# Performance work log

Hardware: AMD Instinct MI355X
Metric: run time of the kernel (lower is better)

## Reference

```python
import jax, jax.numpy as jnp
import numpy as np

V, E, H, C = 50257, 256, 512, 16  # vocab, embed_dim, hidden_size, n_cells
B, T = 256, 128
LN_EPS = 1e-5


def setup_inputs() -> dict:
    key = jax.random.key(0)
    ks = jax.random.split(key, 16)
    s_h = 1.0 / np.sqrt(H)
    s_e = 1.0 / np.sqrt(E)
    return {
        "tokens": jax.random.randint(ks[0], (B, T), 0, V),
        "emb": jax.random.normal(ks[1], (V, E), jnp.float32) * 0.02,
        "Wproj": jax.random.normal(ks[2], (E, H), jnp.float32) * s_e,
        "bproj": jnp.zeros((H,), jnp.float32),
        "Wp": jax.random.normal(ks[3], (C, H, H), jnp.float32) * s_h,
        "bp": jnp.zeros((C, H), jnp.float32),
        "ln_g": jnp.ones((C, H), jnp.float32),
        "ln_b": jnp.zeros((C, H), jnp.float32),
        "Wih": jax.random.normal(ks[4], (C, 4 * H, H), jnp.float32) * s_h,
        "bih": jnp.zeros((C, 4 * H), jnp.float32),
        "Whh": jax.random.normal(ks[5], (C, 4 * H, H), jnp.float32) * s_h,
        "bhh": jnp.zeros((C, 4 * H), jnp.float32),
        "Wa": jax.random.normal(ks[6], (C, H, H), jnp.float32) * s_h,
        "ba": jnp.zeros((C, H), jnp.float32),
        "gate_logit": jnp.zeros((C,), jnp.float32),  # torch.tensor(0.0) per cell
    }


def _layernorm(x, g, b):
    mu = jnp.mean(x, axis=-1, keepdims=True)
    var = jnp.var(x, axis=-1, keepdims=True)
    return (x - mu) * jax.lax.rsqrt(var + LN_EPS) * g + b


def reference(tokens, emb, Wproj, bproj, Wp, bp, ln_g, ln_b,
              Wih, bih, Whh, bhh, Wa, ba, gate_logit):
    # embedding (padding_idx=0 zeroed) + projection to hidden size
    emb = emb.at[0].set(0.0)
    xs = emb[tokens] @ Wproj + bproj              # [B,T,H]
    xs = jnp.transpose(xs, (1, 0, 2))             # [T,B,H] for scan

    gate = jax.nn.sigmoid(gate_logit)[:, None, None]  # [C,1,1]

    def step(carry, x_t):
        h, c, ext = carry                          # h,c: [C,B,H], ext: [B,H]
        # input_adapter == Identity (input_size == hidden_size); external injection
        x = x_t[None] + 0.3 * ext[None]            # [C,B,H]
        # perception: Linear + ReLU + LayerNorm
        p = jax.nn.relu(jnp.einsum('cbh,chk->cbk', x, Wp) + bp[:, None, :])
        p = _layernorm(p, ln_g[:, None, :], ln_b[:, None, :])
        # LSTMCell (torch gate order i, f, g, o)
        gates = (jnp.einsum('cbh,cgh->cbg', p, Wih) + bih[:, None, :]
                 + jnp.einsum('cbh,cgh->cbg', h, Whh) + bhh[:, None, :])
        i_g, f_g, g_g, o_g = jnp.split(gates, 4, axis=-1)
        c_new = jax.nn.sigmoid(f_g) * c + jax.nn.sigmoid(i_g) * jnp.tanh(g_g)
        h_new = jax.nn.sigmoid(o_g) * jnp.tanh(c_new)
        # association + sigmoid gate
        a = jnp.tanh(jnp.einsum('cbh,chk->cbk', h_new, Wa) + ba[:, None, :])
        out = a * gate                             # [C,B,H]
        y = jnp.mean(out, axis=0)                  # aggregate cells -> [B,H]
        return (h_new, c_new, y), y

    h0 = jnp.zeros((C, B, H), xs.dtype)
    c0 = jnp.zeros((C, B, H), xs.dtype)
    ext0 = jnp.zeros((B, H), xs.dtype)
    _, ys = jax.lax.scan(step, (h0, c0, ext0), xs)  # ys: [T,B,H]
    return jnp.transpose(ys, (1, 0, 2))             # [B,T,H]
```

## Files before the change

kernel.cpp:

```cpp
#include <hip/hip_runtime.h>
#include <hip/hip_bf16.h>

#define V 50257
#define E 256
#define H 512
#define C 16
#define B 256
#define T 128

typedef _Float16 f16x8 __attribute__((ext_vector_type(8)));
typedef _Float16 f16x4 __attribute__((ext_vector_type(4)));
typedef float f32x4 __attribute__((ext_vector_type(4)));

__device__ __forceinline__ float sigm(float x) { return 1.0f / (1.0f + __expf(-x)); }

__device__ __forceinline__ void gload16(const _Float16* g, _Float16* l) {
  __builtin_amdgcn_global_load_lds((const __attribute__((address_space(1))) unsigned*)g,
                                   (__attribute__((address_space(3))) unsigned*)l, 16, 0, 0);
}

__global__ __launch_bounds__(256) void k_emb(const int* __restrict__ tokens,
                                             const float* __restrict__ emb,
                                             const float* __restrict__ Wproj,
                                             const float* __restrict__ bproj,
                                             _Float16* __restrict__ xs_h) {
  __shared__ float elds[16][256];
  const int tid = threadIdx.x;
  const int r0 = blockIdx.x * 16;
#pragma unroll
  for (int i = 0; i < 16; ++i) {
    int r = r0 + i;
    int t = r >> 8, b = r & 255;
    int tok = tokens[b * T + t];
    elds[i][tid] = (tok == 0) ? 0.0f : emb[(size_t)tok * E + tid];
  }
  __syncthreads();
  float acc0[16], acc1[16];
#pragma unroll
  for (int i = 0; i < 16; ++i) { acc0[i] = 0.0f; acc1[i] = 0.0f; }
  for (int k = 0; k < E; k += 4) {
    float w0[4], w1[4];
#pragma unroll
    for (int kk = 0; kk < 4; ++kk) {
      w0[kk] = Wproj[(k + kk) * H + tid];
      w1[kk] = Wproj[(k + kk) * H + tid + 256];
    }
#pragma unroll
    for (int i = 0; i < 16; ++i) {
      float4 e4 = *(const float4*)&elds[i][k];
      acc0[i] = fmaf(e4.x, w0[0], acc0[i]);
      acc0[i] = fmaf(e4.y, w0[1], acc0[i]);
      acc0[i] = fmaf(e4.z, w0[2], acc0[i]);
      acc0[i] = fmaf(e4.w, w0[3], acc0[i]);
      acc1[i] = fmaf(e4.x, w1[0], acc1[i]);
      acc1[i] = fmaf(e4.y, w1[1], acc1[i]);
      acc1[i] = fmaf(e4.z, w1[2], acc1[i]);
      acc1[i] = fmaf(e4.w, w1[3], acc1[i]);
    }
  }
  float bp0 = bproj[tid], bp1 = bproj[tid + 256];
#pragma unroll
  for (int i = 0; i < 16; ++i) {
    size_t r = (size_t)(r0 + i);
    xs_h[r * H + tid] = (_Float16)(acc0[i] + bp0);
    xs_h[r * H + tid + 256] = (_Float16)(acc1[i] + bp1);
  }
}

__global__ __launch_bounds__(256) void k_cvt_wg(const float* __restrict__ Wih,
                                                const float* __restrict__ Whh,
                                                _Float16* __restrict__ WgT) {
  for (size_t i4 = ((size_t)blockIdx.x * 256 + threadIdx.x) * 4; i4 < (size_t)33554432;
       i4 += (size_t)gridDim.x * 1024) {
    size_t c = i4 >> 21;
    size_t rem = i4 & 2097151;
    size_t np = rem >> 10;
    size_t k2 = rem & 1023;
    int gate = (int)((np >> 4) & 3);
    int hh = (int)(((np >> 6) << 4) | (np & 15));
    size_t n = (size_t)gate * 512 + hh;
    const float* src = (k2 < 512) ? (Wih + (c * 2048 + n) * 512 + k2)
                                  : (Whh + (c * 2048 + n) * 512 + (k2 - 512));
    float4 v = *(const float4*)src;
    f16x4 o;
    o[0] = (_Float16)v.x; o[1] = (_Float16)v.y; o[2] = (_Float16)v.z; o[3] = (_Float16)v.w;
    *(f16x4*)&WgT[i4] = o;
  }
}

__global__ __launch_bounds__(256) void k_cvt_tr(const float* __restrict__ W,
                                                _Float16* __restrict__ WT) {
  __shared__ float tl[64][65];
  const int tid = threadIdx.x;
  const int c = blockIdx.z;
  const int k0 = blockIdx.y * 64, n0 = blockIdx.x * 64;
  const float* Wc = W + (size_t)c * 262144;
#pragma unroll
  for (int q = 0; q < 16; ++q) {
    int idx = q * 256 + tid;
    int r = idx >> 6, cc = idx & 63;
    tl[r][cc] = Wc[(size_t)(k0 + r) * 512 + n0 + cc];
  }
  __syncthreads();
  _Float16* WTc = WT + (size_t)c * 262144;
#pragma unroll
  for (int q = 0; q < 16; ++q) {
    int idx = q * 256 + tid;
    int rr = idx >> 6, cc = idx & 63;
    WTc[(size_t)(n0 + rr) * 512 + k0 + cc] = (_Float16)tl[cc][rr];
  }
}

__global__ __launch_bounds__(256) void k_bias(const float* __restrict__ bih,
                                              const float* __restrict__ bhh,
                                              float* __restrict__ bsum) {
  int i = blockIdx.x * 256 + threadIdx.x;
  if (i < C * 4 * H) {
    int c = i >> 11, np = i & 2047;
    int gate = (np >> 4) & 3;
    int hh = ((np >> 6) << 4) | (np & 15);
    int n = gate * 512 + hh;
    bsum[i] = bih[c * 2048 + n] + bhh[c * 2048 + n];
  }
}

template <int EPI, int KK, int LDA, int LDB, int ACS, int BCS, int OLD, int BLD>
__global__ __launch_bounds__(256, 2) void k_gemm(const _Float16* __restrict__ A,
                                                 const _Float16* __restrict__ Bm,
                                                 _Float16* __restrict__ hout,
                                                 const float* __restrict__ bias,
                                                 const float* __restrict__ gl,
                                                 float* __restrict__ cstate,
                                                 _Float16* __restrict__ hdst) {
  __shared__ _Float16 Asl[128 * 64];
  __shared__ _Float16 Bsl[128 * 64];
  const int tid = threadIdx.x;
  const int w = tid >> 6, l = tid & 63;
  const int c = blockIdx.z;
  const int m0 = blockIdx.y * 128, n0 = blockIdx.x * 128;
  const _Float16* Ab = A + (size_t)c * ACS + (size_t)m0 * LDA;
  const _Float16* Bb = Bm + (size_t)c * BCS + (size_t)n0 * LDB;
  f32x4 acc[4][4];
#pragma unroll
  for (int i = 0; i < 4; ++i)
#pragma unroll
    for (int j = 0; j < 4; ++j) acc[i][j] = (f32x4)0.0f;
  const int wm = (w >> 1) * 64, wn = (w & 1) * 64;
  const int srow = l >> 3, sj = l & 7;
#pragma unroll 1
  for (int kb = 0; kb < KK / 64; ++kb) {
#pragma unroll
    for (int q = 0; q < 4; ++q) {
      int r = w * 32 + q * 8 + srow;
      int gj = sj ^ (r & 7);
      gload16(Ab + (size_t)r * LDA + kb * 64 + gj * 8, &Asl[(w * 32 + q * 8) * 64]);
      gload16(Bb + (size_t)r * LDB + kb * 64 + gj * 8, &Bsl[(w * 32 + q * 8) * 64]);
    }
    __syncthreads();
#pragma unroll
    for (int s2 = 0; s2 < 2; ++s2) {
      f16x8 af[4], bf[4];
#pragma unroll
      for (int i = 0; i < 4; ++i) {
        int R = wm + i * 16 + (l & 15);
        int p = (s2 * 4 + (l >> 4)) ^ (R & 7);
        af[i] = *(const f16x8*)&Asl[R * 64 + p * 8];
        int RN = wn + i * 16 + (l & 15);
        int pn = (s2 * 4 + (l >> 4)) ^ (RN & 7);
        bf[i] = *(const f16x8*)&Bsl[RN * 64 + pn * 8];
      }
#pragma unroll
      for (int i = 0; i < 4; ++i)
#pragma unroll
        for (int j = 0; j < 4; ++j)
          acc[i][j] = __builtin_amdgcn_mfma_f32_16x16x32_f16(af[i], bf[j], acc[i][j], 0, 0, 0);
    }
    __syncthreads();
  }
  const int rl = (l >> 4) * 4, cl = l & 15;
  if (EPI == 3) {
    const int hh = (((n0 + wn) >> 6) << 4) + cl;
    float bv[4];
#pragma unroll
    for (int j = 0; j < 4; ++j) bv[j] = bias[(size_t)c * BLD + (n0 + wn) + j * 16 + cl];
#pragma unroll
    for (int i = 0; i < 4; ++i) {
#pragma unroll
      for (int rg = 0; rg < 4; ++rg) {
        int row = m0 + wm + i * 16 + rl + rg;
        float ig = acc[i][0][rg] + bv[0];
        float fg = acc[i][1][rg] + bv[1];
        float gg = acc[i][2][rg] + bv[2];
        float og = acc[i][3][rg] + bv[3];
        size_t ci = ((size_t)c * 256 + row) * 512 + hh;
        float cn = sigm(fg) * cstate[ci] + sigm(ig) * tanhf(gg);
        cstate[ci] = cn;
        hdst[((size_t)c * 256 + row) * 1024 + 512 + hh] = (_Float16)(sigm(og) * tanhf(cn));
      }
    }
  } else {
    float gv = 0.0f;
    if (EPI == 2) gv = sigm(gl[c]);
#pragma unroll
    for (int i = 0; i < 4; ++i) {
#pragma unroll
      for (int j = 0; j < 4; ++j) {
        int gc = n0 + wn + j * 16 + cl;
        float bv = bias[(size_t)c * BLD + gc];
#pragma unroll
        for (int rg = 0; rg < 4; ++rg) {
          int gr = m0 + wm + i * 16 + rl + rg;
          float v = acc[i][j][rg] + bv;
          if (EPI == 0) v = fmaxf(v, 0.0f);
          if (EPI == 2) v = tanhf(v) * gv;
          hout[(size_t)c * (256 * (size_t)OLD) + (size_t)gr * OLD + gc] = (_Float16)v;
        }
      }
    }
  }
}

__global__ __launch_bounds__(256) void k_ln(_Float16* __restrict__ Aq,
                                            const float* __restrict__ g,
                                            const float* __restrict__ b) {
  int row = blockIdx.x * 4 + (threadIdx.x >> 6);
  int l = threadIdx.x & 63;
  int c = row >> 8;
  _Float16* p = Aq + (size_t)row * 1024 + l * 8;
  f16x8 v = *(const f16x8*)p;
  float vf[8];
  float s1 = 0.0f, s2 = 0.0f;
#pragma unroll
  for (int j = 0; j < 8; ++j) {
    vf[j] = (float)v[j];
    s1 += vf[j];
    s2 += vf[j] * vf[j];
  }
#pragma unroll
  for (int m = 1; m < 64; m <<= 1) {
    s1 += __shfl_xor(s1, m, 64);
    s2 += __shfl_xor(s2, m, 64);
  }
  float mu = s1 * (1.0f / 512.0f);
  float var = s2 * (1.0f / 512.0f) - mu * mu;
  float rs = rsqrtf(var + 1e-5f);
  int col0 = l * 8;
#pragma unroll
  for (int j = 0; j < 8; ++j) {
    float o = (vf[j] - mu) * rs * g[c * 512 + col0 + j] + b[c * 512 + col0 + j];
    v[j] = (_Float16)o;
  }
  *(f16x8*)p = v;
}

__global__ __launch_bounds__(256) void k_agg(const _Float16* __restrict__ abuf,
                                             const _Float16* __restrict__ xs_h,
                                             _Float16* __restrict__ xq,
                                             float* __restrict__ out, int t) {
  int idx = blockIdx.x * 256 + threadIdx.x;
  int i4 = idx * 4;
  float s[4] = {0.0f, 0.0f, 0.0f, 0.0f};
#pragma unroll
  for (int c = 0; c < 16; ++c) {
    f16x4 a = *(const f16x4*)&abuf[(size_t)c * 131072 + i4];
#pragma unroll
    for (int j = 0; j < 4; ++j) s[j] += (float)a[j];
  }
  int b = i4 >> 9, h = i4 & 511;
  float4 y4;
  float* yp = &y4.x;
#pragma unroll
  for (int j = 0; j < 4; ++j) yp[j] = s[j] * (1.0f / 16.0f);
  *(float4*)&out[((size_t)b * T + t) * 512 + h] = y4;
  if (t + 1 < T) {
    f16x4 xs4 = *(const f16x4*)&xs_h[(size_t)(t + 1) * 131072 + i4];
    f16x4 xn;
#pragma unroll
    for (int j = 0; j < 4; ++j) xn[j] = (_Float16)((float)xs4[j] + 0.3f * yp[j]);
    *(f16x4*)&xq[i4] = xn;
  }
}

extern "C" void kernel_launch(void* const* d_in, const int* in_sizes, int n_in,
                              void* d_out, int out_size, void* d_ws, size_t ws_size,
                              hipStream_t stream) {
  const int* tokens = (const int*)d_in[0];
  const float* emb = (const float*)d_in[1];
  const float* Wproj = (const float*)d_in[2];
  const float* bproj = (const float*)d_in[3];
  const float* Wp = (const float*)d_in[4];
  const float* bp = (const float*)d_in[5];
  const float* ln_g = (const float*)d_in[6];
  const float* ln_b = (const float*)d_in[7];
  const float* Wih = (const float*)d_in[8];
  const float* bih = (const float*)d_in[9];
  const float* Whh = (const float*)d_in[10];
  const float* bhh = (const float*)d_in[11];
  const float* Wa = (const float*)d_in[12];
  const float* ba = (const float*)d_in[13];
  const float* gl = (const float*)d_in[14];
  float* out = (float*)d_out;

  char* w8 = (char*)d_ws;
  _Float16* xs_h = (_Float16*)w8;
  _Float16* Aq0 = (_Float16*)(w8 + 33554432);
  _Float16* Aq1 = (_Float16*)(w8 + 50331648);
  float* cbuf = (float*)(w8 + 67108864);
  _Float16* abuf = (_Float16*)(w8 + 75497472);
  _Float16* xq = (_Float16*)(w8 + 79691776);
  _Float16* WpT = (_Float16*)(w8 + 79953920);
  _Float16* WaT = (_Float16*)(w8 + 88342528);
  _Float16* WgT = (_Float16*)(w8 + 96731136);
  float* bsum = (float*)(w8 + 163840000);

  hipMemsetAsync(Aq0, 0, 16777216, stream);
  hipMemsetAsync(cbuf, 0, 8388608, stream);

  k_cvt_wg<<<4096, 256, 0, stream>>>(Wih, Whh, WgT);
  k_cvt_tr<<<dim3(8, 8, 16), 256, 0, stream>>>(Wp, WpT);
  k_cvt_tr<<<dim3(8, 8, 16), 256, 0, stream>>>(Wa, WaT);
  k_bias<<<128, 256, 0, stream>>>(bih, bhh, bsum);
  k_emb<<<T * B / 16, 256, 0, stream>>>(tokens, emb, Wproj, bproj, xs_h);
  hipMemcpyAsync(xq, xs_h, 262144, hipMemcpyDeviceToDevice, stream);

  for (int t = 0; t < T; ++t) {
    _Float16* Ac = (t & 1) ? Aq1 : Aq0;
    _Float16* An = (t & 1) ? Aq0 : Aq1;
    k_gemm<0, 512, 512, 512, 0, 262144, 1024, 512>
        <<<dim3(4, 2, 16), 256, 0, stream>>>(xq, WpT, Ac, bp, nullptr, nullptr, nullptr);
    k_ln<<<1024, 256, 0, stream>>>(Ac, ln_g, ln_b);
    k_gemm<3, 1024, 1024, 1024, 262144, 2097152, 1, 2048>
        <<<dim3(16, 2, 16), 256, 0, stream>>>(Ac, WgT, nullptr, bsum, nullptr, cbuf, An);
    k_gemm<2, 512, 1024, 512, 262144, 262144, 512, 512>
        <<<dim3(4, 2, 16), 256, 0, stream>>>(An + 512, WaT, abuf, ba, gl, nullptr, nullptr);
    k_agg<<<128, 256, 0, stream>>>(abuf, xs_h, xq, out, t);
  }
}
```

Baseline: 7.975 ms.

## Fuse LayerNorm into perception GEMM and cell aggregation into association GEMM

Perception now uses one kernel, k_pln. Each block computes a full 32x512 row tile of the ReLU projection and applies LayerNorm in the epilogue: row statistics are reduced with shuffles and shared memory. The association GEMM now does the cross-cell mean, the output write and the next-step input injection. The last block to finish each output tile, tracked by a per-step atomic counter, does this work. Together these cut five launches per timestep to three and remove separate passes over the intermediate buffers. The cost is larger per-block tiles, a threadfence plus atomic handshake, and counters stored in the already-consumed t=0 slice of the embedding buffer.

```diff
diff --git a/kernel.cpp b/kernel.cpp
--- a/kernel.cpp
+++ b/kernel.cpp
@@ -124,22 +124,158 @@
   }
 }
 
-template <int EPI, int KK, int LDA, int LDB, int ACS, int BCS, int OLD, int BLD>
-__global__ __launch_bounds__(256, 2) void k_gemm(const _Float16* __restrict__ A,
-                                                 const _Float16* __restrict__ Bm,
-                                                 _Float16* __restrict__ hout,
-                                                 const float* __restrict__ bias,
-                                                 const float* __restrict__ gl,
-                                                 float* __restrict__ cstate,
-                                                 _Float16* __restrict__ hdst) {
+__global__ __launch_bounds__(256, 2) void k_pln(const _Float16* __restrict__ xq,
+                                                const _Float16* __restrict__ WpT,
+                                                const float* __restrict__ bp,
+                                                const float* __restrict__ ln_g,
+                                                const float* __restrict__ ln_b,
+                                                _Float16* __restrict__ Pdst) {
+  __shared__ _Float16 Bsl[512 * 64];
+  const int tid = threadIdx.x;
+  const int w = tid >> 6, l = tid & 63;
+  const int mt = blockIdx.x;
+  const int c = blockIdx.y;
+  const int m0 = mt * 32;
+  const _Float16* Bb = WpT + (size_t)c * 262144;
+  const int srow = l >> 3, sj = l & 7;
+  const int lm = l & 15, lk = l >> 4;
+  f32x4 acc[2][8];
+#pragma unroll
+  for (int i = 0; i < 2; ++i)
+#pragma unroll
+    for (int j = 0; j < 8; ++j) acc[i][j] = (f32x4)0.0f;
+  const _Float16* pA0 = xq + (size_t)(m0 + lm) * 512 + lk * 8;
+  const _Float16* pA1 = pA0 + 16 * 512;
+  f16x8 a0s0 = *(const f16x8*)pA0;
+  f16x8 a0s1 = *(const f16x8*)(pA0 + 32);
+  f16x8 a1s0 = *(const f16x8*)pA1;
+  f16x8 a1s1 = *(const f16x8*)(pA1 + 32);
+#pragma unroll 1
+  for (int kb = 0; kb < 8; ++kb) {
+#pragma unroll
+    for (int q = 0; q < 16; ++q) {
+      int r = q * 32 + w * 8 + srow;
+      int gj = sj ^ (r & 7);
+      gload16(Bb + (size_t)r * 512 + kb * 64 + gj * 8, &Bsl[(q * 32 + w * 8) * 64]);
+    }
+    f16x8 u00 = a0s0, u01 = a0s1, u10 = a1s0, u11 = a1s1;
+    if (kb < 7) {
+      a0s0 = *(const f16x8*)(pA0 + (kb + 1) * 64);
+      a0s1 = *(const f16x8*)(pA0 + (kb + 1) * 64 + 32);
+      a1s0 = *(const f16x8*)(pA1 + (kb + 1) * 64);
+      a1s1 = *(const f16x8*)(pA1 + (kb + 1) * 64 + 32);
+    }
+    __syncthreads();
+#pragma unroll
+    for (int s2 = 0; s2 < 2; ++s2) {
+      f16x8 bf[8];
+#pragma unroll
+      for (int j = 0; j < 8; ++j) {
+        int RN = w * 128 + j * 16 + lm;
+        int pn = (s2 * 4 + lk) ^ (RN & 7);
+        bf[j] = *(const f16x8*)&Bsl[RN * 64 + pn * 8];
+      }
+      f16x8 ua = s2 ? u01 : u00;
+      f16x8 ub = s2 ? u11 : u10;
+#pragma unroll
+      for (int j = 0; j < 8; ++j) {
+        acc[0][j] = __builtin_amdgcn_mfma_f32_16x16x32_f16(ua, bf[j], acc[0][j], 0, 0, 0);
+        acc[1][j] = __builtin_amdgcn_mfma_f32_16x16x32_f16(ub, bf[j], acc[1][j], 0, 0, 0);
+      }
+    }
+    __syncthreads();
+  }
+  float bv[8], gcol[8], bcol[8];
+#pragma unroll
+  for (int j = 0; j < 8; ++j) {
+    int col = w * 128 + j * 16 + lm;
+    bv[j] = bp[c * 512 + col];
+    gcol[j] = ln_g[c * 512 + col];
+    bcol[j] = ln_b[c * 512 + col];
+  }
+  float vals[2][8][4];
+  float s1l[2][4], s2l[2][4];
+#pragma unroll
+  for (int i = 0; i < 2; ++i)
+#pragma unroll
+    for (int rg = 0; rg < 4; ++rg) { s1l[i][rg] = 0.0f; s2l[i][rg] = 0.0f; }
+#pragma unroll
+  for (int i = 0; i < 2; ++i)
+#pragma unroll
+    for (int j = 0; j < 8; ++j)
+#pragma unroll
+      for (int rg = 0; rg < 4; ++rg) {
+        float v = fmaxf(acc[i][j][rg] + bv[j], 0.0f);
+        vals[i][j][rg] = v;
+        s1l[i][rg] += v;
+        s2l[i][rg] += v * v;
+      }
+#pragma unroll
+  for (int m = 1; m < 16; m <<= 1) {
+#pragma unroll
+    for (int i = 0; i < 2; ++i)
+#pragma unroll
+      for (int rg = 0; rg < 4; ++rg) {
+        s1l[i][rg] += __shfl_xor(s1l[i][rg], m, 64);
+        s2l[i][rg] += __shfl_xor(s2l[i][rg], m, 64);
+      }
+  }
+  float* st = (float*)Bsl;
+  if (lm == 0) {
+#pragma unroll
+    for (int i = 0; i < 2; ++i)
+#pragma unroll
+      for (int rg = 0; rg < 4; ++rg) {
+        int row = i * 16 + lk * 4 + rg;
+        st[(w * 32 + row) * 2] = s1l[i][rg];
+        st[(w * 32 + row) * 2 + 1] = s2l[i][rg];
+      }
+  }
+  __syncthreads();
+  float mu_[2][4], rs_[2][4];
+#pragma unroll
+  for (int i = 0; i < 2; ++i)
+#pragma unroll
+    for (int rg = 0; rg < 4; ++rg) {
+      int row = i * 16 + lk * 4 + rg;
+      float t1 = 0.0f, t2 = 0.0f;
+#pragma unroll
+      for (int ww = 0; ww < 4; ++ww) {
+        t1 += st[(ww * 32 + row) * 2];
+        t2 += st[(ww * 32 + row) * 2 + 1];
+      }
+      float mu = t1 * (1.0f / 512.0f);
+      float var = t2 * (1.0f / 512.0f) - mu * mu;
+      mu_[i][rg] = mu;
+      rs_[i][rg] = rsqrtf(var + 1e-5f);
+    }
+#pragma unroll
+  for (int i = 0; i < 2; ++i)
+#pragma unroll
+    for (int j = 0; j < 8; ++j) {
+      int col = w * 128 + j * 16 + lm;
+#pragma unroll
+      for (int rg = 0; rg < 4; ++rg) {
+        int row = i * 16 + lk * 4 + rg;
+        float o = (vals[i][j][rg] - mu_[i][rg]) * rs_[i][rg] * gcol[j] + bcol[j];
+        Pdst[((size_t)c * 256 + m0 + row) * 1024 + col] = (_Float16)o;
+      }
+    }
+}
+
+__global__ __launch_bounds__(256, 2) void k_gates(const _Float16* __restrict__ A,
+                                                  const _Float16* __restrict__ Bm,
+                                                  const float* __restrict__ bias,
+                                                  float* __restrict__ cstate,
+                                                  _Float16* __restrict__ hdst) {
   __shared__ _Float16 Asl[128 * 64];
   __shared__ _Float16 Bsl[128 * 64];
   const int tid = threadIdx.x;
   const int w = tid >> 6, l = tid & 63;
   const int c = blockIdx.z;
   const int m0 = blockIdx.y * 128, n0 = blockIdx.x * 128;
-  const _Float16* Ab = A + (size_t)c * ACS + (size_t)m0 * LDA;
-  const _Float16* Bb = Bm + (size_t)c * BCS + (size_t)n0 * LDB;
+  const _Float16* Ab = A + (size_t)c * 262144 + (size_t)m0 * 1024;
+  const _Float16* Bb = Bm + (size_t)c * 2097152 + (size_t)n0 * 1024;
   f32x4 acc[4][4];
 #pragma unroll
   for (int i = 0; i < 4; ++i)
@@ -148,13 +284,13 @@
   const int wm = (w >> 1) * 64, wn = (w & 1) * 64;
   const int srow = l >> 3, sj = l & 7;
 #pragma unroll 1
-  for (int kb = 0; kb < KK / 64; ++kb) {
+  for (int kb = 0; kb < 16; ++kb) {
 #pragma unroll
     for (int q = 0; q < 4; ++q) {
       int r = w * 32 + q * 8 + srow;
       int gj = sj ^ (r & 7);
-      gload16(Ab + (size_t)r * LDA + kb * 64 + gj * 8, &Asl[(w * 32 + q * 8) * 64]);
-      gload16(Bb + (size_t)r * LDB + kb * 64 + gj * 8, &Bsl[(w * 32 + q * 8) * 64]);
+      gload16(Ab + (size_t)r * 1024 + kb * 64 + gj * 8, &Asl[(w * 32 + q * 8) * 64]);
+      gload16(Bb + (size_t)r * 1024 + kb * 64 + gj * 8, &Bsl[(w * 32 + q * 8) * 64]);
     }
     __syncthreads();
 #pragma unroll
@@ -178,106 +314,142 @@
     __syncthreads();
   }
   const int rl = (l >> 4) * 4, cl = l & 15;
-  if (EPI == 3) {
-    const int hh = (((n0 + wn) >> 6) << 4) + cl;
-    float bv[4];
-#pragma unroll
-    for (int j = 0; j < 4; ++j) bv[j] = bias[(size_t)c * BLD + (n0 + wn) + j * 16 + cl];
-#pragma unroll
-    for (int i = 0; i < 4; ++i) {
+  const int hh = (((n0 + wn) >> 6) << 4) + cl;
+  float bv[4];
+#pragma unroll
+  for (int j = 0; j < 4; ++j) bv[j] = bias[(size_t)c * 2048 + (n0 + wn) + j * 16 + cl];
+#pragma unroll
+  for (int i = 0; i < 4; ++i) {
+#pragma unroll
+    for (int rg = 0; rg < 4; ++rg) {
+      int row = m0 + wm + i * 16 + rl + rg;
+      float ig = acc[i][0][rg] + bv[0];
+      float fg = acc[i][1][rg] + bv[1];
+      float gg = acc[i][2][rg] + bv[2];
+      float og = acc[i][3][rg] + bv[3];
+      size_t ci = ((size_t)c * 256 + row) * 512 + hh;
+      float cn = sigm(fg) * cstate[ci] + sigm(ig) * tanhf(gg);
+      cstate[ci] = cn;
+      hdst[((size_t)c * 256 + row) * 1024 + 512 + hh] = (_Float16)(sigm(og) * tanhf(cn));
+    }
+  }
+}
+
+__global__ __launch_bounds__(256, 2) void k_assoc(const _Float16* __restrict__ An,
+                                                  const _Float16* __restrict__ WaT,
+                                                  const float* __restrict__ ba,
+                                                  const float* __restrict__ gl,
+                                                  _Float16* __restrict__ abuf,
+                                                  unsigned* __restrict__ cnt,
+                                                  const _Float16* __restrict__ xs_h,
+                                                  _Float16* __restrict__ xq,
+                                                  float* __restrict__ out, int t) {
+  __shared__ _Float16 Asl[64 * 64];
+  __shared__ _Float16 Bsl[128 * 64];
+  __shared__ int lastFlag;
+  const int tid = threadIdx.x;
+  const int w = tid >> 6, l = tid & 63;
+  const int nt = blockIdx.x, mt = blockIdx.y, c = blockIdx.z;
+  const int n0 = nt * 128;
+  const _Float16* Ab = An + 512 + ((size_t)c * 256 + mt * 64) * 1024;
+  const _Float16* Bb = WaT + (size_t)c * 262144 + (size_t)n0 * 512;
+  f32x4 acc[2][4];
+#pragma unroll
+  for (int i = 0; i < 2; ++i)
+#pragma unroll
+    for (int j = 0; j < 4; ++j) acc[i][j] = (f32x4)0.0f;
+  const int wm = (w >> 1) * 32, wn = (w & 1) * 64;
+  const int srow = l >> 3, sj = l & 7;
+  const int lm = l & 15, lk = l >> 4;
+#pragma unroll 1
+  for (int kb = 0; kb < 8; ++kb) {
+#pragma unroll
+    for (int q = 0; q < 2; ++q) {
+      int r = q * 32 + w * 8 + srow;
+      int gj = sj ^ (r & 7);
+      gload16(Ab + (size_t)r * 1024 + kb * 64 + gj * 8, &Asl[(q * 32 + w * 8) * 64]);
+    }
+#pragma unroll
+    for (int q = 0; q < 4; ++q) {
+      int r = q * 32 + w * 8 + srow;
+      int gj = sj ^ (r & 7);
+      gload16(Bb + (size_t)r * 512 + kb * 64 + gj * 8, &Bsl[(q * 32 + w * 8) * 64]);
+    }
+    __syncthreads();
+#pragma unroll
+    for (int s2 = 0; s2 < 2; ++s2) {
+      f16x8 af[2], bf[4];
+#pragma unroll
+      for (int i = 0; i < 2; ++i) {
+        int R = wm + i * 16 + lm;
+        int p = (s2 * 4 + lk) ^ (R & 7);
+        af[i] = *(const f16x8*)&Asl[R * 64 + p * 8];
+      }
+#pragma unroll
+      for (int j = 0; j < 4; ++j) {
+        int RN = wn + j * 16 + lm;
+        int pn = (s2 * 4 + lk) ^ (RN & 7);
+        bf[j] = *(const f16x8*)&Bsl[RN * 64 + pn * 8];
+      }
+#pragma unroll
+      for (int i = 0; i < 2; ++i)
+#pragma unroll
+        for (int j = 0; j < 4; ++j)
+          acc[i][j] = __builtin_amdgcn_mfma_f32_16x16x32_f16(af[i], bf[j], acc[i][j], 0, 0, 0);
+    }
+    __syncthreads();
+  }
+  float gv = sigm(gl[c]);
+#pragma unroll
+  for (int i = 0; i < 2; ++i)
+#pragma unroll
+    for (int j = 0; j < 4; ++j) {
+      int gc = n0 + wn + j * 16 + lm;
+      float bav = ba[c * 512 + gc];
 #pragma unroll
       for (int rg = 0; rg < 4; ++rg) {
-        int row = m0 + wm + i * 16 + rl + rg;
-        float ig = acc[i][0][rg] + bv[0];
-        float fg = acc[i][1][rg] + bv[1];
-        float gg = acc[i][2][rg] + bv[2];
-        float og = acc[i][3][rg] + bv[3];
-        size_t ci = ((size_t)c * 256 + row) * 512 + hh;
-        float cn = sigm(fg) * cstate[ci] + sigm(ig) * tanhf(gg);
-        cstate[ci] = cn;
-        hdst[((size_t)c * 256 + row) * 1024 + 512 + hh] = (_Float16)(sigm(og) * tanhf(cn));
-      }
-    }
-  } else {
-    float gv = 0.0f;
-    if (EPI == 2) gv = sigm(gl[c]);
-#pragma unroll
-    for (int i = 0; i < 4; ++i) {
-#pragma unroll
-      for (int j = 0; j < 4; ++j) {
-        int gc = n0 + wn + j * 16 + cl;
-        float bv = bias[(size_t)c * BLD + gc];
-#pragma unroll
-        for (int rg = 0; rg < 4; ++rg) {
-          int gr = m0 + wm + i * 16 + rl + rg;
-          float v = acc[i][j][rg] + bv;
-          if (EPI == 0) v = fmaxf(v, 0.0f);
-          if (EPI == 2) v = tanhf(v) * gv;
-          hout[(size_t)c * (256 * (size_t)OLD) + (size_t)gr * OLD + gc] = (_Float16)v;
-        }
-      }
-    }
-  }
-}
-
-__global__ __launch_bounds__(256) void k_ln(_Float16* __restrict__ Aq,
-                                            const float* __restrict__ g,
-                                            const float* __restrict__ b) {
-  int row = blockIdx.x * 4 + (threadIdx.x >> 6);
-  int l = threadIdx.x & 63;
-  int c = row >> 8;
-  _Float16* p = Aq + (size_t)row * 1024 + l * 8;
-  f16x8 v = *(const f16x8*)p;
-  float vf[8];
-  float s1 = 0.0f, s2 = 0.0f;
-#pragma unroll
-  for (int j = 0; j < 8; ++j) {
-    vf[j] = (float)v[j];
-    s1 += vf[j];
-    s2 += vf[j] * vf[j];
-  }
-#pragma unroll
-  for (int m = 1; m < 64; m <<= 1) {
-    s1 += __shfl_xor(s1, m, 64);
-    s2 += __shfl_xor(s2, m, 64);
-  }
-  float mu = s1 * (1.0f / 512.0f);
-  float var = s2 * (1.0f / 512.0f) - mu * mu;
-  float rs = rsqrtf(var + 1e-5f);
-  int col0 = l * 8;
-#pragma unroll
-  for (int j = 0; j < 8; ++j) {
-    float o = (vf[j] - mu) * rs * g[c * 512 + col0 + j] + b[c * 512 + col0 + j];
-    v[j] = (_Float16)o;
-  }
-  *(f16x8*)p = v;
-}
-
-__global__ __launch_bounds__(256) void k_agg(const _Float16* __restrict__ abuf,
-                                             const _Float16* __restrict__ xs_h,
-                                             _Float16* __restrict__ xq,
-                                             float* __restrict__ out, int t) {
-  int idx = blockIdx.x * 256 + threadIdx.x;
-  int i4 = idx * 4;
-  float s[4] = {0.0f, 0.0f, 0.0f, 0.0f};
-#pragma unroll
-  for (int c = 0; c < 16; ++c) {
-    f16x4 a = *(const f16x4*)&abuf[(size_t)c * 131072 + i4];
-#pragma unroll
-    for (int j = 0; j < 4; ++j) s[j] += (float)a[j];
-  }
-  int b = i4 >> 9, h = i4 & 511;
-  float4 y4;
-  float* yp = &y4.x;
-#pragma unroll
-  for (int j = 0; j < 4; ++j) yp[j] = s[j] * (1.0f / 16.0f);
-  *(float4*)&out[((size_t)b * T + t) * 512 + h] = y4;
-  if (t + 1 < T) {
-    f16x4 xs4 = *(const f16x4*)&xs_h[(size_t)(t + 1) * 131072 + i4];
-    f16x4 xn;
-#pragma unroll
-    for (int j = 0; j < 4; ++j) xn[j] = (_Float16)((float)xs4[j] + 0.3f * yp[j]);
-    *(f16x4*)&xq[i4] = xn;
+        int row = mt * 64 + wm + i * 16 + lk * 4 + rg;
+        float v = tanhf(acc[i][j][rg] + bav) * gv;
+        abuf[(size_t)c * 131072 + (size_t)row * 512 + gc] = (_Float16)v;
+      }
+    }
+  __threadfence();
+  __syncthreads();
+  if (tid == 0) {
+    unsigned old = atomicAdd(&cnt[t * 16 + mt * 4 + nt], 1u);
+    lastFlag = (old == 15u);
+  }
+  __syncthreads();
+  if (!lastFlag) return;
+  __threadfence();
+  const int br0 = mt * 64;
+#pragma unroll 1
+  for (int rnd = 0; rnd < 4; ++rnd) {
+    int g = rnd * 256 + tid;
+    int row = g >> 4;
+    int colg = (g & 15) * 8;
+    size_t off = (size_t)(br0 + row) * 512 + n0 + colg;
+    float s[8] = {0, 0, 0, 0, 0, 0, 0, 0};
+#pragma unroll
+    for (int cc = 0; cc < 16; ++cc) {
+      f16x8 a = *(const f16x8*)&abuf[(size_t)cc * 131072 + off];
+#pragma unroll
+      for (int j = 0; j < 8; ++j) s[j] += (float)a[j];
+    }
+    float y[8];
+#pragma unroll
+    for (int j = 0; j < 8; ++j) y[j] = s[j] * (1.0f / 16.0f);
+    int b = br0 + row, hcol = n0 + colg;
+    float* op = &out[((size_t)b * T + t) * 512 + hcol];
+    *(float4*)op = make_float4(y[0], y[1], y[2], y[3]);
+    *(float4*)(op + 4) = make_float4(y[4], y[5], y[6], y[7]);
+    if (t + 1 < T) {
+      f16x8 xs4 = *(const f16x8*)&xs_h[(size_t)(t + 1) * 131072 + off];
+      f16x8 xn;
+#pragma unroll
+      for (int j = 0; j < 8; ++j) xn[j] = (_Float16)((float)xs4[j] + 0.3f * y[j]);
+      *(f16x8*)&xq[off] = xn;
+    }
   }
 }
 
@@ -312,6 +484,7 @@
   _Float16* WaT = (_Float16*)(w8 + 88342528);
   _Float16* WgT = (_Float16*)(w8 + 96731136);
   float* bsum = (float*)(w8 + 163840000);
+  unsigned* cnt = (unsigned*)w8;
 
   hipMemsetAsync(Aq0, 0, 16777216, stream);
   hipMemsetAsync(cbuf, 0, 8388608, stream);
@@ -322,17 +495,13 @@
   k_bias<<<128, 256, 0, stream>>>(bih, bhh, bsum);
   k_emb<<<T * B / 16, 256, 0, stream>>>(tokens, emb, Wproj, bproj, xs_h);
   hipMemcpyAsync(xq, xs_h, 262144, hipMemcpyDeviceToDevice, stream);
+  hipMemsetAsync(cnt, 0, 8192, stream);
 
   for (int t = 0; t < T; ++t) {
     _Float16* Ac = (t & 1) ? Aq1 : Aq0;
     _Float16* An = (t & 1) ? Aq0 : Aq1;
-    k_gemm<0, 512, 512, 512, 0, 262144, 1024, 512>
-        <<<dim3(4, 2, 16), 256, 0, stream>>>(xq, WpT, Ac, bp, nullptr, nullptr, nullptr);
-    k_ln<<<1024, 256, 0, stream>>>(Ac, ln_g, ln_b);
-    k_gemm<3, 1024, 1024, 1024, 262144, 2097152, 1, 2048>
-        <<<dim3(16, 2, 16), 256, 0, stream>>>(Ac, WgT, nullptr, bsum, nullptr, cbuf, An);
-    k_gemm<2, 512, 1024, 512, 262144, 262144, 512, 512>
-        <<<dim3(4, 2, 16), 256, 0, stream>>>(An + 512, WaT, abuf, ba, gl, nullptr, nullptr);
-    k_agg<<<128, 256, 0, stream>>>(abuf, xs_h, xq, out, t);
-  }
-}
+    k_pln<<<dim3(8, 16), 256, 0, stream>>>(xq, WpT, bp, ln_g, ln_b, Ac);
+    k_gates<<<dim3(16, 2, 16), 256, 0, stream>>>(Ac, WgT, bsum, cbuf, An);
+    k_assoc<<<dim3(4, 4, 16), 256, 0, stream>>>(An, WaT, ba, gl, abuf, cnt, xs_h, xq, out, t);
+  }
+}
```

Measured after the change: 12.03 ms. 1.51x slower.
